# Optimization experiments

Hardware: AMD Instinct MI355X
Metric: run time of the kernel (lower is better)

Reference implementation:

```python
import jax, jax.numpy as jnp
import numpy as np

B, S, D, H = 4, 2048, 1024, 16
DK = D // H


def setup_inputs() -> dict:
    key = jax.random.key(0)
    ks = jax.random.split(key, 10)
    s = 0.02  # keep linear outputs well-scaled
    causal = jnp.triu(jnp.ones((S, S), dtype=bool), k=1)  # True = masked
    return {
        "Q": jax.random.normal(ks[0], (B, S, D), dtype=jnp.float32),
        "K_V": jax.random.normal(ks[1], (B, S, D), dtype=jnp.float32),
        "mask": jnp.broadcast_to(causal, (B, S, S)),
        "Wq": jax.random.normal(ks[2], (D, D), dtype=jnp.float32) * s,
        "bq": jnp.zeros((D,), dtype=jnp.float32),
        "Wk": jax.random.normal(ks[3], (D, D), dtype=jnp.float32) * s,
        "bk": jnp.zeros((D,), dtype=jnp.float32),
        "Wv": jax.random.normal(ks[4], (D, D), dtype=jnp.float32) * s,
        "bv": jnp.zeros((D,), dtype=jnp.float32),
        "Wo": jax.random.normal(ks[5], (D, D), dtype=jnp.float32) * s,
        "bo": jnp.zeros((D,), dtype=jnp.float32),
    }


def reference(Q, K_V, mask, Wq, bq, Wk, bk, Wv, bv, Wo, bo):
    # Linear projections
    q = Q @ Wq + bq          # [B, Sq, D]
    k = K_V @ Wk + bk        # [B, Sk, D]
    v = K_V @ Wv + bv        # [B, Sk, D]
    Sq, Sk = q.shape[1], k.shape[1]
    # chunk(dim=2)+cat(dim=0) == split into H heads of size DK
    q = q.reshape(B, Sq, H, DK)
    k = k.reshape(B, Sk, H, DK)
    v = v.reshape(B, Sk, H, DK)
    scale = 1.0 / jnp.sqrt(jnp.float32(DK))
    scores = jnp.einsum("bqhd,bkhd->bhqk", q, k) * scale  # [B,H,Sq,Sk]
    # mask.repeat(head_num,1,1) == broadcast mask over heads
    scores = jnp.where(mask[:, None, :, :], -jnp.inf, scores)
    attn = jax.nn.softmax(scores, axis=-1)
    # dropout is identity in eval mode
    out = jnp.einsum("bhqk,bkhd->bqhd", attn, v).reshape(B, Sq, D)
    return out @ Wo + bo
```

## Files before the change

kernel.cpp:

```cpp
#include <hip/hip_runtime.h>

typedef unsigned short u16;
typedef __attribute__((ext_vector_type(8))) __bf16 bf16x8;
typedef __attribute__((ext_vector_type(4))) float f32x4;

#define B_  4
#define S_  2048
#define D_  1024
#define H_  16
#define DK_ 64

__device__ __forceinline__ u16 f2bf(float f) {
  unsigned u = __float_as_uint(f);
  u += 0x7fffu + ((u >> 16) & 1u);
  return (u16)(u >> 16);
}
__device__ __forceinline__ float hexp2(float f) {
  return __builtin_amdgcn_exp2f(f);
}
__device__ __forceinline__ unsigned pack_bf2(float f0, float f1) {
  return __builtin_amdgcn_perm(__float_as_uint(f1), __float_as_uint(f0), 0x07060302u);
}

__device__ __forceinline__ void load_lds16(const u16* g, u16* l) {
  __builtin_amdgcn_global_load_lds((const __attribute__((address_space(1))) void*)g,
                                   (__attribute__((address_space(3))) void*)l,
                                   16, 0, 0);
}

__global__ void cvt_bf16_2(const float* __restrict__ x0, u16* __restrict__ y0,
                           const float* __restrict__ x1, u16* __restrict__ y1, int n4) {
  int i = blockIdx.x * blockDim.x + threadIdx.x;
  const float* x = x0; u16* y = y0;
  int j = i;
  if (i >= n4) { x = x1; y = y1; j = i - n4; }
  float4 v = ((const float4*)x)[j];
  ushort4 o;
  o.x = f2bf(v.x); o.y = f2bf(v.y); o.z = f2bf(v.z); o.w = f2bf(v.w);
  ((ushort4*)y)[j] = o;
}

__global__ void transpose_cvt4(const float* __restrict__ W0, const float* __restrict__ W1,
                               const float* __restrict__ W2, const float* __restrict__ W3,
                               u16* __restrict__ T0, u16* __restrict__ T1,
                               u16* __restrict__ T2, u16* __restrict__ T3) {
  __shared__ float tile[32][33];
  const float* W = (blockIdx.z == 0) ? W0 : (blockIdx.z == 1) ? W1 : (blockIdx.z == 2) ? W2 : W3;
  u16*         T = (blockIdx.z == 0) ? T0 : (blockIdx.z == 1) ? T1 : (blockIdx.z == 2) ? T2 : T3;
  int bx = blockIdx.x * 32, by = blockIdx.y * 32;
  int tx = threadIdx.x, ty = threadIdx.y;
  #pragma unroll
  for (int i = 0; i < 32; i += 8)
    tile[ty + i][tx] = W[(size_t)(by + ty + i) * D_ + bx + tx];
  __syncthreads();
  #pragma unroll
  for (int i = 0; i < 32; i += 8)
    T[(size_t)(bx + ty + i) * D_ + by + tx] = f2bf(tile[tx][ty + i]);
}

#define GBM 128
#define GBN 256
#define GNT 16

template<int MODE>
__global__ __launch_bounds__(512, 2)
void gemm8p(const u16* __restrict__ Aq, const u16* __restrict__ Ak,
            const u16* __restrict__ Bt,
            const float* __restrict__ bq, const float* __restrict__ bk,
            const float* __restrict__ bv,
            u16* __restrict__ qp, u16* __restrict__ kp, u16* __restrict__ vpT,
            float* __restrict__ Cf, float qscale) {
  __shared__ __align__(16) u16 sm[2 * 24576];
  const int tid  = threadIdx.x;
  const int lane = tid & 63, wave = tid >> 6;
  const int bm = blockIdx.x * GBM;
  const int bn = blockIdx.y * GBN;
  const int wm = (wave >> 2) * 64, wn = (wave & 3) * 64;
  const int fm = lane & 15, fk4 = lane >> 4;
  const int K = D_;

  int path = 0;
  const u16* A = Aq;
  if constexpr (MODE == 0) { path = bn >> 10; if (path != 0) A = Ak; }

  const int sr  = tid >> 2;
  const int sl  = tid & 3;
  const int kof = sl * 8;
  const u16* gA  = A  + (size_t)(bm + sr) * K + kof;
  const u16* gB0 = Bt + (size_t)(bn + sr) * K + kof;
  const u16* gB1 = Bt + (size_t)(bn + 128 + sr) * K + kof;

#define GR(t, ks) do { \
    u16* lr_ = &sm[((t) & 1) * 24576 + (ks) * 12288]; \
    const int ko_ = (t) * 64 + (ks) * 32; \
    load_lds16(gA  + ko_, lr_ + tid * 8); \
    load_lds16(gB0 + ko_, lr_ + 4096 + tid * 8); \
    load_lds16(gB1 + ko_, lr_ + 8192 + tid * 8); \
  } while (0)

  f32x4 acc[4][4] = {};

  GR(0, 0);
  asm volatile("" ::: "memory");
  GR(0, 1);
  asm volatile("" ::: "memory");
  GR(1, 0);

  #pragma unroll
  for (int t = 0; t < GNT; ++t) {
    #pragma unroll
    for (int ks = 0; ks < 2; ++ks) {
      if (t < GNT - 1)  asm volatile("s_waitcnt vmcnt(6)" ::: "memory");
      else if (ks == 0) asm volatile("s_waitcnt vmcnt(3)" ::: "memory");
      else              asm volatile("s_waitcnt vmcnt(0)" ::: "memory");
      __builtin_amdgcn_s_barrier();
      if (ks == 0) { if (t + 1 < GNT) GR(t + 1, 1); }
      else         { if (t + 2 < GNT) GR(t + 2, 0); }
      asm volatile("" ::: "memory");

      const u16* rb = &sm[(t & 1) * 24576 + ks * 12288];
      bf16x8 af[4], bfr[4];
      #pragma unroll
      for (int m = 0; m < 4; ++m)
        af[m] = *(const bf16x8*)&rb[(wm + m * 16 + fm) * 32 + fk4 * 8];
      #pragma unroll
      for (int j = 0; j < 4; ++j)
        bfr[j] = *(const bf16x8*)&rb[(128 + wn + j * 16 + fm) * 32 + fk4 * 8];
      __builtin_amdgcn_s_setprio(1);
      #pragma unroll
      for (int m = 0; m < 4; ++m)
        #pragma unroll
        for (int j = 0; j < 4; ++j)
          acc[m][j] = __builtin_amdgcn_mfma_f32_16x16x32_bf16(af[m], bfr[j], acc[m][j], 0, 0, 0);
      __builtin_amdgcn_s_setprio(0);
    }
  }
#undef GR

  if constexpr (MODE == 0) {
    #pragma unroll
    for (int i = 0; i < 4; ++i) {
      #pragma unroll
      for (int j = 0; j < 4; ++j) {
        int colg = bn + wn + j * 16 + fm;
        int rowg0 = bm + wm + i * 16 + fk4 * 4;
        if (path == 0) {
          float bb = bq[colg];
          #pragma unroll
          for (int rg = 0; rg < 4; ++rg)
            qp[(size_t)(rowg0 + rg) * D_ + colg] = f2bf((acc[i][j][rg] + bb) * qscale);
        } else if (path == 1) {
          int ck = colg - 1024;
          float bb = bk[ck];
          #pragma unroll
          for (int rg = 0; rg < 4; ++rg)
            kp[(size_t)(rowg0 + rg) * D_ + ck] = f2bf(acc[i][j][rg] + bb);
        } else {
          int cv = colg - 2048;
          float bb = bv[cv];
          int hh = cv >> 6, dk = cv & 63;
          int bbt = rowg0 >> 11, s = rowg0 & (S_ - 1);
          ushort4 pk4;
          pk4.x = f2bf(acc[i][j][0] + bb);
          pk4.y = f2bf(acc[i][j][1] + bb);
          pk4.z = f2bf(acc[i][j][2] + bb);
          pk4.w = f2bf(acc[i][j][3] + bb);
          *(ushort4*)&vpT[(((size_t)bbt * H_ + hh) * DK_ + dk) * S_ + s] = pk4;
        }
      }
    }
  } else {
    #pragma unroll
    for (int i = 0; i < 4; ++i)
      #pragma unroll
      for (int j = 0; j < 4; ++j) {
        int colg = bn + wn + j * 16 + fm;
        float bb = bq[colg];
        #pragma unroll
        for (int rg = 0; rg < 4; ++rg) {
          int rowg = bm + wm + i * 16 + fk4 * 4 + rg;
          Cf[(size_t)rowg * D_ + colg] = acc[i][j][rg] + bb;
        }
      }
  }
}

__global__ __launch_bounds__(256, 2)
void attn_kernel(const u16* __restrict__ qp, const u16* __restrict__ kp,
                 const u16* __restrict__ vpT, u16* __restrict__ ao) {
  __shared__ u16 Ks[2][16 * 512];
  __shared__ u16 Vs[2][16 * 512];
  __shared__ u16 Ps[4 * 4 * 512];

  const int tid  = threadIdx.x;
  const int lane = tid & 63;
  const int w    = tid >> 6;
  const int fm   = lane & 15;
  const int fk4  = lane >> 4;
  const int csl  = (lane ^ ((lane >> 3) & 7)) * 8;

  const int i  = blockIdx.x;
  const int qt = 15 - (i >> 6);
  const int bh = i & 63;
  const int b  = bh >> 4;
  const int h  = bh & 15;

  const int q0 = qt * 128 + w * 32;
  const int nj = qt + 1;

  u16* Pw = &Ps[w * 2048];
  const u16* kb = kp  + (size_t)(b * S_) * D_ + h * DK_;
  const u16* vb = vpT + (size_t)((b * H_ + h) * DK_) * S_;

#define STAGEKV(bf, jj) do { \
    const int kv0_ = (jj) * 128; \
    _Pragma("unroll") \
    for (int c = 0; c < 4; ++c) { \
      int idx = 4 * w + c; \
      load_lds16(kb + (size_t)(kv0_ + (idx >> 1) * 16 + fm) * D_ + (idx & 1) * 32 + fk4 * 8, \
                 &Ks[bf][idx * 512 + lane * 8]); \
    } \
    _Pragma("unroll") \
    for (int c = 0; c < 4; ++c) { \
      int idx = 4 * w + c; \
      load_lds16(vb + (size_t)((idx & 3) * 16 + fm) * S_ + kv0_ + (idx >> 2) * 32 + fk4 * 8, \
                 &Vs[bf][idx * 512 + lane * 8]); \
    } } while (0)

  bf16x8 aq[2][2];
  #pragma unroll
  for (int qf = 0; qf < 2; ++qf)
    #pragma unroll
    for (int kh = 0; kh < 2; ++kh)
      aq[qf][kh] = *(const bf16x8*)(qp + (size_t)(b * S_ + q0 + qf * 16 + fm) * D_
                                       + h * DK_ + kh * 32 + fk4 * 8);

  f32x4 oacc[2][4] = {};
  float l0 = 0.f, l1 = 0.f;

  STAGEKV(0, 0);

  #pragma unroll 1
  for (int j = 0; j < nj; ++j) {
    const int kv0 = j * 128;
    const bool lastt = (j == qt);

    __builtin_amdgcn_s_barrier();
    if (j + 1 < nj) {
      STAGEKV((j + 1) & 1, j + 1);
      asm volatile("s_waitcnt vmcnt(8)" ::: "memory");
    } else {
      asm volatile("s_waitcnt vmcnt(0)" ::: "memory");
    }
    __builtin_amdgcn_s_barrier();

    const u16* Kb_ = &Ks[j & 1][0];
    const u16* Vb_ = &Vs[j & 1][0];

    #pragma unroll
    for (int h2 = 0; h2 < 2; ++h2) {
      #pragma unroll
      for (int mtl = 0; mtl < 4; ++mtl) {
        const int mt = h2 * 4 + mtl;
        bf16x8 kf0 = *(const bf16x8*)&Kb_[(mt * 2 + 0) * 512 + lane * 8];
        bf16x8 kf1 = *(const bf16x8*)&Kb_[(mt * 2 + 1) * 512 + lane * 8];
        f32x4 z0 = {0.f, 0.f, 0.f, 0.f}, z1 = z0;
        __builtin_amdgcn_s_setprio(1);
        z0 = __builtin_amdgcn_mfma_f32_16x16x32_bf16(kf0, aq[0][0], z0, 0, 0, 0);
        z0 = __builtin_amdgcn_mfma_f32_16x16x32_bf16(kf1, aq[0][1], z0, 0, 0, 0);
        z1 = __builtin_amdgcn_mfma_f32_16x16x32_bf16(kf0, aq[1][0], z1, 0, 0, 0);
        z1 = __builtin_amdgcn_mfma_f32_16x16x32_bf16(kf1, aq[1][1], z1, 0, 0, 0);
        __builtin_amdgcn_s_setprio(0);

        const int kvr = kv0 + mt * 16 + fk4 * 4;
        float e0[4], e1[4];
        #pragma unroll
        for (int rg = 0; rg < 4; ++rg) {
          float zz0 = z0[rg], zz1 = z1[rg];
          if (lastt) {
            if (kvr + rg > q0 + fm)      zz0 = -1e30f;
            if (kvr + rg > q0 + 16 + fm) zz1 = -1e30f;
          }
          e0[rg] = hexp2(zz0);
          e1[rg] = hexp2(zz1);
          l0 += e0[rg]; l1 += e1[rg];
        }
        const int ktl  = mtl >> 1;
        const int fk4c = (mt & 1) * 2 + (fk4 >> 1);
        const int c    = fk4c * 16 + fm;
        const int woff = (c ^ ((c >> 3) & 7)) * 8 + (fk4 & 1) * 4;
        uint2 w0, w1;
        w0.x = pack_bf2(e0[0], e0[1]); w0.y = pack_bf2(e0[2], e0[3]);
        w1.x = pack_bf2(e1[0], e1[1]); w1.y = pack_bf2(e1[2], e1[3]);
        *(uint2*)&Pw[(ktl * 2 + 0) * 512 + woff] = w0;
        *(uint2*)&Pw[(ktl * 2 + 1) * 512 + woff] = w1;
      }

      #pragma unroll
      for (int ktl = 0; ktl < 2; ++ktl) {
        const int kt = h2 * 2 + ktl;
        bf16x8 ap0 = *(const bf16x8*)&Pw[(ktl * 2 + 0) * 512 + csl];
        bf16x8 ap1 = *(const bf16x8*)&Pw[(ktl * 2 + 1) * 512 + csl];
        __builtin_amdgcn_s_setprio(1);
        #pragma unroll
        for (int nt = 0; nt < 4; ++nt) {
          bf16x8 bv = *(const bf16x8*)&Vb_[(kt * 4 + nt) * 512 + lane * 8];
          oacc[0][nt] = __builtin_amdgcn_mfma_f32_16x16x32_bf16(ap0, bv, oacc[0][nt], 0, 0, 0);
          oacc[1][nt] = __builtin_amdgcn_mfma_f32_16x16x32_bf16(ap1, bv, oacc[1][nt], 0, 0, 0);
        }
        __builtin_amdgcn_s_setprio(0);
      }
    }
  }
#undef STAGEKV

  #pragma unroll
  for (int qf = 0; qf < 2; ++qf) {
    float ls = (qf == 0) ? l0 : l1;
    ls += __shfl_xor(ls, 16, 64);
    ls += __shfl_xor(ls, 32, 64);
    #pragma unroll
    for (int rg = 0; rg < 4; ++rg) {
      float lr = __shfl(ls, fk4 * 4 + rg, 64);
      float inv = 1.0f / lr;
      int q = q0 + qf * 16 + fk4 * 4 + rg;
      #pragma unroll
      for (int nt = 0; nt < 4; ++nt) {
        float o = oacc[qf][nt][rg] * inv;
        ao[(size_t)(b * S_ + q) * D_ + h * DK_ + nt * 16 + fm] = f2bf(o);
      }
    }
  }
}

extern "C" void kernel_launch(void* const* d_in, const int* in_sizes, int n_in,
                              void* d_out, int out_size, void* d_ws, size_t ws_size,
                              hipStream_t stream) {
  const float* Q  = (const float*)d_in[0];
  const float* KV = (const float*)d_in[1];
  const float* Wq = (const float*)d_in[3];
  const float* bq = (const float*)d_in[4];
  const float* Wk = (const float*)d_in[5];
  const float* bk = (const float*)d_in[6];
  const float* Wv = (const float*)d_in[7];
  const float* bv = (const float*)d_in[8];
  const float* Wo = (const float*)d_in[9];
  const float* bo = (const float*)d_in[10];
  float* out = (float*)d_out;

  char* ws = (char*)d_ws;
  u16* Qb  = (u16*)(ws);
  u16* Kb  = (u16*)(ws + (16ull << 20));
  u16* Wqt = (u16*)(ws + (32ull << 20));
  u16* Wkt = (u16*)(ws + (34ull << 20));
  u16* Wvt = (u16*)(ws + (36ull << 20));
  u16* Wot = (u16*)(ws + (38ull << 20));
  u16* qp  = (u16*)(ws + (40ull << 20));
  u16* kp  = (u16*)(ws + (56ull << 20));
  u16* vpT = (u16*)(ws + (72ull << 20));
  u16* ao  = Qb;

  const int n4 = (B_ * S_ * D_) / 4;
  cvt_bf16_2<<<2 * n4 / 256, 256, 0, stream>>>(Q, Qb, KV, Kb, n4);

  transpose_cvt4<<<dim3(32, 32, 4), dim3(32, 8), 0, stream>>>(Wq, Wk, Wv, Wo,
                                                              Wqt, Wkt, Wvt, Wot);

  const float qscale = 0.125f * 1.44269504f;
  gemm8p<0><<<dim3(8192 / GBM, 3072 / GBN), 512, 0, stream>>>(
      Qb, Kb, Wqt, bq, bk, bv, qp, kp, vpT, nullptr, qscale);

  attn_kernel<<<1024, 256, 0, stream>>>(qp, kp, vpT, ao);

  gemm8p<1><<<dim3(8192 / GBM, 1024 / GBN), 512, 0, stream>>>(
      ao, nullptr, Wot, bo, nullptr, nullptr, nullptr, nullptr, nullptr, out, 1.0f);
}
```

Measured before the change: 321.9 us.

## Halve attention tiles, pair causal q-tiles per block, compute row sums via MFMA

The attention kernel now uses 64-row query and key/value tiles with 16 query rows per wave, which shrinks shared memory and lets launch bounds target 4 blocks per CU. Each block handles a short and a long causal q-tile (p and 31-p), so every block does similar work and the grid is better balanced. The softmax row sums are computed with an extra MFMA against a vector of ones instead of scalar adds plus shuffles. The trade-off is less K/V reuse per loaded tile, more barriers per unit of work, and an extra MFMA per step, in exchange for higher occupancy and a smaller tail.

```diff
diff --git a/kernel.cpp b/kernel.cpp
--- a/kernel.cpp
+++ b/kernel.cpp
@@ -185,12 +185,12 @@
   }
 }
 
-__global__ __launch_bounds__(256, 2)
+__global__ __launch_bounds__(256, 4)
 void attn_kernel(const u16* __restrict__ qp, const u16* __restrict__ kp,
                  const u16* __restrict__ vpT, u16* __restrict__ ao) {
-  __shared__ u16 Ks[2][16 * 512];
-  __shared__ u16 Vs[2][16 * 512];
-  __shared__ u16 Ps[4 * 4 * 512];
+  __shared__ u16 Ks[2][8 * 512];
+  __shared__ u16 Vs[2][8 * 512];
+  __shared__ u16 Ps[4][512];
 
   const int tid  = threadIdx.x;
   const int lane = tid & 63;
@@ -199,138 +199,122 @@
   const int fk4  = lane >> 4;
   const int csl  = (lane ^ ((lane >> 3) & 7)) * 8;
 
-  const int i  = blockIdx.x;
-  const int qt = 15 - (i >> 6);
+  const int i = blockIdx.x;
+  const int p = i >> 6;
   const int bh = i & 63;
   const int b  = bh >> 4;
   const int h  = bh & 15;
 
-  const int q0 = qt * 128 + w * 32;
-  const int nj = qt + 1;
-
-  u16* Pw = &Ps[w * 2048];
   const u16* kb = kp  + (size_t)(b * S_) * D_ + h * DK_;
   const u16* vb = vpT + (size_t)((b * H_ + h) * DK_) * S_;
 
+  bf16x8 vones;
+  #pragma unroll
+  for (int e = 0; e < 8; ++e) vones[e] = (__bf16)1.0f;
+
 #define STAGEKV(bf, jj) do { \
-    const int kv0_ = (jj) * 128; \
+    const int kv0_ = (jj) * 64; \
     _Pragma("unroll") \
-    for (int c = 0; c < 4; ++c) { \
-      int idx = 4 * w + c; \
+    for (int c = 0; c < 2; ++c) { \
+      int idx = 2 * w + c;                    \
       load_lds16(kb + (size_t)(kv0_ + (idx >> 1) * 16 + fm) * D_ + (idx & 1) * 32 + fk4 * 8, \
                  &Ks[bf][idx * 512 + lane * 8]); \
     } \
     _Pragma("unroll") \
-    for (int c = 0; c < 4; ++c) { \
-      int idx = 4 * w + c; \
+    for (int c = 0; c < 2; ++c) { \
+      int idx = 2 * w + c;                    \
       load_lds16(vb + (size_t)((idx & 3) * 16 + fm) * S_ + kv0_ + (idx >> 2) * 32 + fk4 * 8, \
                  &Vs[bf][idx * 512 + lane * 8]); \
     } } while (0)
 
-  bf16x8 aq[2][2];
-  #pragma unroll
-  for (int qf = 0; qf < 2; ++qf)
+  #pragma unroll 1
+  for (int sidx = 0; sidx < 2; ++sidx) {
+    const int qt = (sidx == 0) ? p : 31 - p;
+    const int q0 = qt * 64 + w * 16;
+    const int nj = qt + 1;
+
+    bf16x8 aq[2];
     #pragma unroll
     for (int kh = 0; kh < 2; ++kh)
-      aq[qf][kh] = *(const bf16x8*)(qp + (size_t)(b * S_ + q0 + qf * 16 + fm) * D_
-                                       + h * DK_ + kh * 32 + fk4 * 8);
-
-  f32x4 oacc[2][4] = {};
-  float l0 = 0.f, l1 = 0.f;
-
-  STAGEKV(0, 0);
-
-  #pragma unroll 1
-  for (int j = 0; j < nj; ++j) {
-    const int kv0 = j * 128;
-    const bool lastt = (j == qt);
+      aq[kh] = *(const bf16x8*)(qp + (size_t)(b * S_ + q0 + fm) * D_
+                                   + h * DK_ + kh * 32 + fk4 * 8);
+
+    f32x4 oacc[4] = {};
+    f32x4 lacc = {0.f, 0.f, 0.f, 0.f};
 
     __builtin_amdgcn_s_barrier();
-    if (j + 1 < nj) {
-      STAGEKV((j + 1) & 1, j + 1);
-      asm volatile("s_waitcnt vmcnt(8)" ::: "memory");
-    } else {
-      asm volatile("s_waitcnt vmcnt(0)" ::: "memory");
-    }
-    __builtin_amdgcn_s_barrier();
-
-    const u16* Kb_ = &Ks[j & 1][0];
-    const u16* Vb_ = &Vs[j & 1][0];
-
-    #pragma unroll
-    for (int h2 = 0; h2 < 2; ++h2) {
-      #pragma unroll
-      for (int mtl = 0; mtl < 4; ++mtl) {
-        const int mt = h2 * 4 + mtl;
-        bf16x8 kf0 = *(const bf16x8*)&Kb_[(mt * 2 + 0) * 512 + lane * 8];
-        bf16x8 kf1 = *(const bf16x8*)&Kb_[(mt * 2 + 1) * 512 + lane * 8];
-        f32x4 z0 = {0.f, 0.f, 0.f, 0.f}, z1 = z0;
-        __builtin_amdgcn_s_setprio(1);
-        z0 = __builtin_amdgcn_mfma_f32_16x16x32_bf16(kf0, aq[0][0], z0, 0, 0, 0);
-        z0 = __builtin_amdgcn_mfma_f32_16x16x32_bf16(kf1, aq[0][1], z0, 0, 0, 0);
-        z1 = __builtin_amdgcn_mfma_f32_16x16x32_bf16(kf0, aq[1][0], z1, 0, 0, 0);
-        z1 = __builtin_amdgcn_mfma_f32_16x16x32_bf16(kf1, aq[1][1], z1, 0, 0, 0);
-        __builtin_amdgcn_s_setprio(0);
-
-        const int kvr = kv0 + mt * 16 + fk4 * 4;
-        float e0[4], e1[4];
+    STAGEKV(0, 0);
+
+    #pragma unroll 1
+    for (int j = 0; j < nj; ++j) {
+      const int kv0 = j * 64;
+      const bool lastt = (j == nj - 1);
+
+      __builtin_amdgcn_s_barrier();
+      if (j + 1 < nj) {
+        STAGEKV((j + 1) & 1, j + 1);
+        asm volatile("s_waitcnt vmcnt(4)" ::: "memory");
+      } else {
+        asm volatile("s_waitcnt vmcnt(0)" ::: "memory");
+      }
+      __builtin_amdgcn_s_barrier();
+
+      const u16* Kb_ = &Ks[j & 1][0];
+      const u16* Vb_ = &Vs[j & 1][0];
+
+      #pragma unroll
+      for (int kth = 0; kth < 2; ++kth) {
         #pragma unroll
-        for (int rg = 0; rg < 4; ++rg) {
-          float zz0 = z0[rg], zz1 = z1[rg];
-          if (lastt) {
-            if (kvr + rg > q0 + fm)      zz0 = -1e30f;
-            if (kvr + rg > q0 + 16 + fm) zz1 = -1e30f;
+        for (int mtl = 0; mtl < 2; ++mtl) {
+          const int mt = kth * 2 + mtl;
+          bf16x8 kf0 = *(const bf16x8*)&Kb_[(mt * 2 + 0) * 512 + lane * 8];
+          bf16x8 kf1 = *(const bf16x8*)&Kb_[(mt * 2 + 1) * 512 + lane * 8];
+          f32x4 z = {0.f, 0.f, 0.f, 0.f};
+          __builtin_amdgcn_s_setprio(1);
+          z = __builtin_amdgcn_mfma_f32_16x16x32_bf16(kf0, aq[0], z, 0, 0, 0);
+          z = __builtin_amdgcn_mfma_f32_16x16x32_bf16(kf1, aq[1], z, 0, 0, 0);
+          __builtin_amdgcn_s_setprio(0);
+
+          const int kvr = kv0 + mt * 16 + fk4 * 4;
+          float e[4];
+          #pragma unroll
+          for (int rg = 0; rg < 4; ++rg) {
+            float zz = z[rg];
+            if (lastt && (kvr + rg > q0 + fm)) zz = -1e30f;
+            e[rg] = hexp2(zz);
           }
-          e0[rg] = hexp2(zz0);
-          e1[rg] = hexp2(zz1);
-          l0 += e0[rg]; l1 += e1[rg];
+          const int fk4c = (mt & 1) * 2 + (fk4 >> 1);
+          const int c    = fk4c * 16 + fm;
+          const int woff = (c ^ ((c >> 3) & 7)) * 8 + (fk4 & 1) * 4;
+          uint2 wv;
+          wv.x = pack_bf2(e[0], e[1]); wv.y = pack_bf2(e[2], e[3]);
+          *(uint2*)&Ps[w][woff] = wv;
         }
-        const int ktl  = mtl >> 1;
-        const int fk4c = (mt & 1) * 2 + (fk4 >> 1);
-        const int c    = fk4c * 16 + fm;
-        const int woff = (c ^ ((c >> 3) & 7)) * 8 + (fk4 & 1) * 4;
-        uint2 w0, w1;
-        w0.x = pack_bf2(e0[0], e0[1]); w0.y = pack_bf2(e0[2], e0[3]);
-        w1.x = pack_bf2(e1[0], e1[1]); w1.y = pack_bf2(e1[2], e1[3]);
-        *(uint2*)&Pw[(ktl * 2 + 0) * 512 + woff] = w0;
-        *(uint2*)&Pw[(ktl * 2 + 1) * 512 + woff] = w1;
-      }
-
-      #pragma unroll
-      for (int ktl = 0; ktl < 2; ++ktl) {
-        const int kt = h2 * 2 + ktl;
-        bf16x8 ap0 = *(const bf16x8*)&Pw[(ktl * 2 + 0) * 512 + csl];
-        bf16x8 ap1 = *(const bf16x8*)&Pw[(ktl * 2 + 1) * 512 + csl];
+
+        bf16x8 ap = *(const bf16x8*)&Ps[w][csl];
         __builtin_amdgcn_s_setprio(1);
         #pragma unroll
         for (int nt = 0; nt < 4; ++nt) {
-          bf16x8 bv = *(const bf16x8*)&Vb_[(kt * 4 + nt) * 512 + lane * 8];
-          oacc[0][nt] = __builtin_amdgcn_mfma_f32_16x16x32_bf16(ap0, bv, oacc[0][nt], 0, 0, 0);
-          oacc[1][nt] = __builtin_amdgcn_mfma_f32_16x16x32_bf16(ap1, bv, oacc[1][nt], 0, 0, 0);
+          bf16x8 bv = *(const bf16x8*)&Vb_[(kth * 4 + nt) * 512 + lane * 8];
+          oacc[nt] = __builtin_amdgcn_mfma_f32_16x16x32_bf16(ap, bv, oacc[nt], 0, 0, 0);
         }
+        lacc = __builtin_amdgcn_mfma_f32_16x16x32_bf16(ap, vones, lacc, 0, 0, 0);
         __builtin_amdgcn_s_setprio(0);
+      }
+    }
+
+    #pragma unroll
+    for (int rg = 0; rg < 4; ++rg) {
+      float inv = 1.0f / lacc[rg];
+      int q = q0 + fk4 * 4 + rg;
+      #pragma unroll
+      for (int nt = 0; nt < 4; ++nt) {
+        float o = oacc[nt][rg] * inv;
+        ao[(size_t)(b * S_ + q) * D_ + h * DK_ + nt * 16 + fm] = f2bf(o);
       }
     }
   }
 #undef STAGEKV
-
-  #pragma unroll
-  for (int qf = 0; qf < 2; ++qf) {
-    float ls = (qf == 0) ? l0 : l1;
-    ls += __shfl_xor(ls, 16, 64);
-    ls += __shfl_xor(ls, 32, 64);
-    #pragma unroll
-    for (int rg = 0; rg < 4; ++rg) {
-      float lr = __shfl(ls, fk4 * 4 + rg, 64);
-      float inv = 1.0f / lr;
-      int q = q0 + qf * 16 + fk4 * 4 + rg;
-      #pragma unroll
-      for (int nt = 0; nt < 4; ++nt) {
-        float o = oacc[qf][nt][rg] * inv;
-        ao[(size_t)(b * S_ + q) * D_ + h * DK_ + nt * 16 + fm] = f2bf(o);
-      }
-    }
-  }
 }
 
 extern "C" void kernel_launch(void* const* d_in, const int* in_sizes, int n_in,
```

Measured after the change: 336.2 us. +4.5%, slower.

## Restructure GEMM to 4 waves with 64x128 warp tiles and triple-buffered K=32 stages

Applied to the files above, without the earlier changes.

The projection GEMMs move from 8 waves (64x64 per wave) to 4 waves (64x128 per wave), doubling each wave's MFMA work and accumulator registers. The pipeline switches from double-buffered 64-wide K chunks split into two sub-steps to a three-stage ring of 32-wide K chunks, with one barrier per stage and six async loads per thread. The goal is more register-level reuse of A fragments and less LDS traffic per MFMA. In exchange, the 128 accumulator VGPRs per thread raise register pressure and fewer waves are available to hide latency.

```diff
diff --git a/kernel.cpp b/kernel.cpp
--- a/kernel.cpp
+++ b/kernel.cpp
@@ -60,22 +60,22 @@
 
 #define GBM 128
 #define GBN 256
-#define GNT 16
+#define GNT 32
 
 template<int MODE>
-__global__ __launch_bounds__(512, 2)
+__global__ __launch_bounds__(256, 2)
 void gemm8p(const u16* __restrict__ Aq, const u16* __restrict__ Ak,
             const u16* __restrict__ Bt,
             const float* __restrict__ bq, const float* __restrict__ bk,
             const float* __restrict__ bv,
             u16* __restrict__ qp, u16* __restrict__ kp, u16* __restrict__ vpT,
             float* __restrict__ Cf, float qscale) {
-  __shared__ __align__(16) u16 sm[2 * 24576];
+  __shared__ __align__(16) u16 sm[3 * 12288];
   const int tid  = threadIdx.x;
   const int lane = tid & 63, wave = tid >> 6;
   const int bm = blockIdx.x * GBM;
   const int bn = blockIdx.y * GBN;
-  const int wm = (wave >> 2) * 64, wn = (wave & 3) * 64;
+  const int wm = (wave >> 1) * 64, wn = (wave & 1) * 128;
   const int fm = lane & 15, fk4 = lane >> 4;
   const int K = D_;
 
@@ -83,57 +83,51 @@
   const u16* A = Aq;
   if constexpr (MODE == 0) { path = bn >> 10; if (path != 0) A = Ak; }
 
-  const int sr  = tid >> 2;
-  const int sl  = tid & 3;
-  const int kof = sl * 8;
-  const u16* gA  = A  + (size_t)(bm + sr) * K + kof;
-  const u16* gB0 = Bt + (size_t)(bn + sr) * K + kof;
-  const u16* gB1 = Bt + (size_t)(bn + 128 + sr) * K + kof;
-
-#define GR(t, ks) do { \
-    u16* lr_ = &sm[((t) & 1) * 24576 + (ks) * 12288]; \
-    const int ko_ = (t) * 64 + (ks) * 32; \
-    load_lds16(gA  + ko_, lr_ + tid * 8); \
-    load_lds16(gB0 + ko_, lr_ + 4096 + tid * 8); \
-    load_lds16(gB1 + ko_, lr_ + 8192 + tid * 8); \
+  const int sr = tid >> 2;
+  const int sl = (tid & 3) * 8;
+  const u16* gA = A  + (size_t)(bm + sr) * K + sl;
+  const u16* gB = Bt + (size_t)(bn + sr) * K + sl;
+
+#define GR(t) do { \
+    u16* d_ = &sm[((t) % 3) * 12288]; \
+    const int ko_ = (t) * 32; \
+    load_lds16(gA + ko_,           d_ + tid * 8); \
+    load_lds16(gA + 64 * K + ko_,  d_ + 2048 + tid * 8); \
+    load_lds16(gB + ko_,           d_ + 4096 + tid * 8); \
+    load_lds16(gB + 64 * K + ko_,  d_ + 6144 + tid * 8); \
+    load_lds16(gB + 128 * K + ko_, d_ + 8192 + tid * 8); \
+    load_lds16(gB + 192 * K + ko_, d_ + 10240 + tid * 8); \
   } while (0)
 
-  f32x4 acc[4][4] = {};
-
-  GR(0, 0);
+  f32x4 acc[4][8] = {};
+
+  GR(0);
   asm volatile("" ::: "memory");
-  GR(0, 1);
-  asm volatile("" ::: "memory");
-  GR(1, 0);
+  GR(1);
 
   #pragma unroll
   for (int t = 0; t < GNT; ++t) {
-    #pragma unroll
-    for (int ks = 0; ks < 2; ++ks) {
-      if (t < GNT - 1)  asm volatile("s_waitcnt vmcnt(6)" ::: "memory");
-      else if (ks == 0) asm volatile("s_waitcnt vmcnt(3)" ::: "memory");
-      else              asm volatile("s_waitcnt vmcnt(0)" ::: "memory");
-      __builtin_amdgcn_s_barrier();
-      if (ks == 0) { if (t + 1 < GNT) GR(t + 1, 1); }
-      else         { if (t + 2 < GNT) GR(t + 2, 0); }
-      asm volatile("" ::: "memory");
-
-      const u16* rb = &sm[(t & 1) * 24576 + ks * 12288];
-      bf16x8 af[4], bfr[4];
-      #pragma unroll
-      for (int m = 0; m < 4; ++m)
-        af[m] = *(const bf16x8*)&rb[(wm + m * 16 + fm) * 32 + fk4 * 8];
-      #pragma unroll
-      for (int j = 0; j < 4; ++j)
-        bfr[j] = *(const bf16x8*)&rb[(128 + wn + j * 16 + fm) * 32 + fk4 * 8];
-      __builtin_amdgcn_s_setprio(1);
-      #pragma unroll
-      for (int m = 0; m < 4; ++m)
-        #pragma unroll
-        for (int j = 0; j < 4; ++j)
-          acc[m][j] = __builtin_amdgcn_mfma_f32_16x16x32_bf16(af[m], bfr[j], acc[m][j], 0, 0, 0);
-      __builtin_amdgcn_s_setprio(0);
-    }
+    if (t < GNT - 1) asm volatile("s_waitcnt vmcnt(6)" ::: "memory");
+    else             asm volatile("s_waitcnt vmcnt(0)" ::: "memory");
+    __builtin_amdgcn_s_barrier();
+    if (t + 2 < GNT) GR(t + 2);
+    asm volatile("" ::: "memory");
+
+    const u16* rb = &sm[(t % 3) * 12288];
+    bf16x8 af[4], bfr[8];
+    #pragma unroll
+    for (int m = 0; m < 4; ++m)
+      af[m] = *(const bf16x8*)&rb[(wm + m * 16 + fm) * 32 + fk4 * 8];
+    #pragma unroll
+    for (int j = 0; j < 8; ++j)
+      bfr[j] = *(const bf16x8*)&rb[(128 + wn + j * 16 + fm) * 32 + fk4 * 8];
+    __builtin_amdgcn_s_setprio(1);
+    #pragma unroll
+    for (int m = 0; m < 4; ++m)
+      #pragma unroll
+      for (int j = 0; j < 8; ++j)
+        acc[m][j] = __builtin_amdgcn_mfma_f32_16x16x32_bf16(af[m], bfr[j], acc[m][j], 0, 0, 0);
+    __builtin_amdgcn_s_setprio(0);
   }
 #undef GR
 
@@ -141,7 +135,7 @@
     #pragma unroll
     for (int i = 0; i < 4; ++i) {
       #pragma unroll
-      for (int j = 0; j < 4; ++j) {
+      for (int j = 0; j < 8; ++j) {
         int colg = bn + wn + j * 16 + fm;
         int rowg0 = bm + wm + i * 16 + fk4 * 4;
         if (path == 0) {
@@ -173,7 +167,7 @@
     #pragma unroll
     for (int i = 0; i < 4; ++i)
       #pragma unroll
-      for (int j = 0; j < 4; ++j) {
+      for (int j = 0; j < 8; ++j) {
         int colg = bn + wn + j * 16 + fm;
         float bb = bq[colg];
         #pragma unroll
@@ -367,11 +361,11 @@
                                                               Wqt, Wkt, Wvt, Wot);
 
   const float qscale = 0.125f * 1.44269504f;
-  gemm8p<0><<<dim3(8192 / GBM, 3072 / GBN), 512, 0, stream>>>(
+  gemm8p<0><<<dim3(8192 / GBM, 3072 / GBN), 256, 0, stream>>>(
       Qb, Kb, Wqt, bq, bk, bv, qp, kp, vpT, nullptr, qscale);
 
   attn_kernel<<<1024, 256, 0, stream>>>(qp, kp, vpT, ao);
 
-  gemm8p<1><<<dim3(8192 / GBM, 1024 / GBN), 512, 0, stream>>>(
+  gemm8p<1><<<dim3(8192 / GBM, 1024 / GBN), 256, 0, stream>>>(
       ao, nullptr, Wot, bo, nullptr, nullptr, nullptr, nullptr, nullptr, out, 1.0f);
 }
```

After: 321.7 us. About the same (-0.1%).
